# Optimization experiments

Measured on AMD Instinct MI355X. Metric: run time of the kernel, lower is better.

The kernel has to match this reference:

```python
import jax, jax.numpy as jnp
import numpy as np
from jax.scipy.special import logsumexp

B, L, S, C = 8, 2048, 2048, 256
ITERS = 20

def setup_inputs() -> dict:
    key = jax.random.key(0)
    k0, k1 = jax.random.split(key)
    feat_c0 = jax.random.normal(k0, (B, L, C), dtype=jnp.float32)
    feat_c1 = jax.random.normal(k1, (B, S, C), dtype=jnp.float32)
    bin_score = jnp.ones((), dtype=jnp.float32)  # init_bin_score = 1.0
    return {"feat_c0": feat_c0, "feat_c1": feat_c1, "bin_score": bin_score}

def _uniform_prior(b, m, n):
    # build_uniform_prior: norm = -log(m+n); log_mu/[log_nu] over augmented rows/cols
    fm, fn = jnp.float32(m), jnp.float32(n)
    norm = -jnp.log(fm + fn)
    log_mu = jnp.concatenate([jnp.full((m,), norm, jnp.float32), (jnp.log(fn) + norm)[None]])
    log_nu = jnp.concatenate([jnp.full((n,), norm, jnp.float32), (jnp.log(fm) + norm)[None]])
    log_mu = jnp.broadcast_to(log_mu[None], (b, m + 1))
    log_nu = jnp.broadcast_to(log_nu[None], (b, n + 1))
    return log_mu, log_nu, norm

def _log_sinkhorn(Z, log_mu, log_nu, iters):
    u0 = jnp.zeros_like(log_mu)
    v0 = jnp.zeros_like(log_nu)
    def body(carry, _):
        u, v = carry
        u = log_mu - logsumexp(Z + v[:, None, :], axis=2)  # [B, M+1]
        v = log_nu - logsumexp(Z + u[:, :, None], axis=1)  # [B, N+1]
        return (u, v), None
    (u, v), _ = jax.lax.scan(body, (u0, v0), None, length=iters)
    return Z + u[:, :, None] + v[:, None, :]

def reference(feat_c0, feat_c1, bin_score):
    b, m, n = feat_c0.shape[0], feat_c0.shape[1], feat_c1.shape[1]
    scores = jnp.einsum('blc,bsc->bls', feat_c0, feat_c1)  # [B, M, N]
    # augment with dustbin row/col
    bins0 = jnp.broadcast_to(bin_score, (b, m, 1))
    bins1 = jnp.broadcast_to(bin_score, (b, 1, n))
    alpha = jnp.broadcast_to(bin_score, (b, 1, 1))
    Zin = jnp.concatenate([
        jnp.concatenate([scores, bins0], axis=-1),
        jnp.concatenate([bins1, alpha], axis=-1),
    ], axis=1)  # [B, M+1, N+1]
    log_mu, log_nu, norm = _uniform_prior(b, m, n)
    Z = _log_sinkhorn(Zin, log_mu, log_nu, ITERS)
    return Z - norm
```

## Files before the change

### kernel.cpp

```cpp
#include <hip/hip_runtime.h>

#define Bn 8
#define Mn 2048
#define Nn 2048
#define Cn 256
#define Np1 2049
#define Mp1 2049
#define UVS 2056
#define SINK_ITERS 20
#define NORM   (-8.3177661667193428f)
#define LOGBIN (-0.6931471805599453f)
#define LOG2E  (1.4426950408889634f)
#define LN2    (0.6931471805599453f)
#define NORM2  (-12.0f)
#define LOGBIN2 (-1.0f)
#define PNORM  (8.3177661667193428f)

#define EXP2(x) __builtin_amdgcn_exp2f(x)
#define LOG2(x) __builtin_amdgcn_logf(x)

typedef __bf16 v8bf __attribute__((ext_vector_type(8)));
typedef float  v4f  __attribute__((ext_vector_type(4)));
typedef unsigned short v8u __attribute__((ext_vector_type(8)));

__device__ __forceinline__ float bf2f(unsigned short h){
  return __uint_as_float(((unsigned)h) << 16);
}
__device__ __forceinline__ unsigned short f2bf(float f){
  unsigned u = __float_as_uint(f);
  return (unsigned short)((u + 0x7FFFu + ((u >> 16) & 1u)) >> 16);
}
__device__ __forceinline__ float ldS(const float* p){ return *p; }
__device__ __forceinline__ float ldS(const unsigned short* p){ return bf2f(*p); }
__device__ __forceinline__ void  stS(float* p, float x){ *p = x; }
__device__ __forceinline__ void  stS(unsigned short* p, float x){ *p = f2bf(x); }

__device__ __forceinline__ void ons(float x, float& m, float& s){
  if (x <= m) { s += __expf(x - m); }
  else        { s = s * __expf(m - x) + 1.0f; m = x; }
}
__device__ __forceinline__ void comb(float& m, float& s, float m2, float s2){
  if (m2 <= m) { s += s2 * __expf(m2 - m); }
  else         { s = s * __expf(m - m2) + s2; m = m2; }
}

__global__ void __launch_bounds__(256) conv_k(
    const float* __restrict__ in, unsigned short* __restrict__ out, float scale)
{
  size_t idx = (size_t)blockIdx.x * 256 + threadIdx.x;
  const float* p = in + idx * 8;
  v4f a = *(const v4f*)p;
  v4f c = *(const v4f*)(p + 4);
  v8u o;
  #pragma unroll
  for (int e = 0; e < 4; ++e){ o[e] = f2bf(a[e] * scale); o[e+4] = f2bf(c[e] * scale); }
  *(v8u*)(out + idx * 8) = o;
}

__global__ void __launch_bounds__(256) gemm_b(
    const unsigned short* __restrict__ A, const unsigned short* __restrict__ Bm,
    unsigned short* __restrict__ S, long srow)
{
  int wid  = (blockIdx.x * 256 + threadIdx.x) >> 6;
  int lane = threadIdx.x & 63;
  int b  = wid >> 10;
  int tt = wid & 1023;
  int i0 = (tt >> 5) << 6;
  int j0 = (tt & 31) << 6;
  int ln = lane & 15, qd = lane >> 4;
  const unsigned short* Ab = A  + (size_t)b * Mn * Cn;
  const unsigned short* Bb = Bm + (size_t)b * Nn * Cn;

  v4f acc[4][4];
  #pragma unroll
  for (int r = 0; r < 4; ++r)
    #pragma unroll
    for (int c = 0; c < 4; ++c)
      #pragma unroll
      for (int e = 0; e < 4; ++e) acc[r][c][e] = 0.0f;

  #pragma unroll
  for (int k0 = 0; k0 < Cn; k0 += 32){
    int kk = k0 + qd * 8;
    v8bf af[4], bfr[4];
    #pragma unroll
    for (int r = 0; r < 4; ++r)
      af[r] = *(const v8bf*)(const void*)(Ab + (size_t)(i0 + r*16 + ln) * Cn + kk);
    #pragma unroll
    for (int c = 0; c < 4; ++c)
      bfr[c] = *(const v8bf*)(const void*)(Bb + (size_t)(j0 + c*16 + ln) * Cn + kk);
    #pragma unroll
    for (int r = 0; r < 4; ++r)
      #pragma unroll
      for (int c = 0; c < 4; ++c)
        acc[r][c] = __builtin_amdgcn_mfma_f32_16x16x32_bf16(af[r], bfr[c], acc[r][c], 0, 0, 0);
  }

  unsigned short* Sb = S + (size_t)b * Mn * Nn;
  #pragma unroll
  for (int r = 0; r < 4; ++r){
    #pragma unroll
    for (int e = 0; e < 4; ++e){
      int row = i0 + r*16 + qd*4 + e;
      #pragma unroll
      for (int c = 0; c < 4; ++c)
        Sb[(size_t)row * srow + (j0 + c*16 + ln)] = f2bf(acc[r][c][e] * LOG2E);
    }
  }
}

__global__ void __launch_bounds__(256) rmax_k(
    const unsigned short* __restrict__ S, float* __restrict__ rmax)
{
  int b = blockIdx.y, lane = threadIdx.x & 63;
  int i = blockIdx.x * 4 + (threadIdx.x >> 6);
  const unsigned short* Sr = S + ((size_t)b * Mn + i) * Nn;
  float m = -3.0e38f;
  #pragma unroll
  for (int q = 0; q < 4; ++q){
    v8u sv = *(const v8u*)(Sr + q * 512 + lane * 8);
    #pragma unroll
    for (int c = 0; c < 8; ++c) m = fmaxf(m, bf2f(sv[c]));
  }
  #pragma unroll
  for (int off = 32; off > 0; off >>= 1) m = fmaxf(m, __shfl_xor(m, off));
  if (lane == 0) rmax[(size_t)b * UVS + i] = m;
}

__global__ void __launch_bounds__(256) pass3_k(
    const unsigned short* __restrict__ S, const float* __restrict__ vin,
    float* __restrict__ uout, const float* __restrict__ rmax,
    const float* __restrict__ binp)
{
  int b = blockIdx.y, t = threadIdx.x;
  const float* vb = vin + (size_t)b * UVS;
  __shared__ float red[8];
  if (blockIdx.x < Mn / 4){
    int lane = t & 63;
    int i = blockIdx.x * 4 + (t >> 6);
    const unsigned short* Sr = S + ((size_t)b * Mn + i) * Nn;
    v4f va[8];
    #pragma unroll
    for (int q = 0; q < 4; ++q){
      int j0 = q * 512 + lane * 8;
      va[2*q]   = *(const v4f*)(vb + j0);
      va[2*q+1] = *(const v4f*)(vb + j0 + 4);
    }
    float mv = va[0][0];
    #pragma unroll
    for (int h = 0; h < 8; ++h)
      #pragma unroll
      for (int e = 0; e < 4; ++e) mv = fmaxf(mv, va[h][e]);
    #pragma unroll
    for (int off = 32; off > 0; off >>= 1) mv = fmaxf(mv, __shfl_xor(mv, off));
    float bin2 = binp[0] * LOG2E;
    float vN = vb[Nn];
    float shift = fmaxf(rmax[(size_t)b * UVS + i] + mv, bin2 + vN);
    #pragma unroll
    for (int h = 0; h < 8; ++h)
      #pragma unroll
      for (int e = 0; e < 4; ++e) va[h][e] -= shift;
    float s0 = 0.f, s1 = 0.f, s2 = 0.f, s3 = 0.f;
    #pragma unroll
    for (int q = 0; q < 4; ++q){
      v8u sv = *(const v8u*)(Sr + q * 512 + lane * 8);
      s0 += EXP2(bf2f(sv[0]) + va[2*q][0]);
      s1 += EXP2(bf2f(sv[1]) + va[2*q][1]);
      s2 += EXP2(bf2f(sv[2]) + va[2*q][2]);
      s3 += EXP2(bf2f(sv[3]) + va[2*q][3]);
      s0 += EXP2(bf2f(sv[4]) + va[2*q+1][0]);
      s1 += EXP2(bf2f(sv[5]) + va[2*q+1][1]);
      s2 += EXP2(bf2f(sv[6]) + va[2*q+1][2]);
      s3 += EXP2(bf2f(sv[7]) + va[2*q+1][3]);
    }
    float s = (s0 + s1) + (s2 + s3);
    #pragma unroll
    for (int off = 32; off > 0; off >>= 1) s += __shfl_xor(s, off);
    if (lane == 0){
      s += EXP2(bin2 + vN - shift);
      uout[(size_t)b * UVS + i] = NORM2 - (shift + LOG2(s));
    }
  } else {
    float x[9];
    #pragma unroll
    for (int k = 0; k < 9; ++k){
      int j = t + k * 256;
      x[k] = (j <= Nn) ? vb[j] : -3.0e38f;
    }
    float m = x[0];
    #pragma unroll
    for (int k = 1; k < 9; ++k) m = fmaxf(m, x[k]);
    #pragma unroll
    for (int off = 32; off > 0; off >>= 1) m = fmaxf(m, __shfl_down(m, off));
    int w = t >> 6;
    if ((t & 63) == 0) red[w] = m;
    __syncthreads();
    float M = fmaxf(fmaxf(red[0], red[1]), fmaxf(red[2], red[3]));
    float s = 0.0f;
    #pragma unroll
    for (int k = 0; k < 9; ++k) s += EXP2(x[k] - M);
    #pragma unroll
    for (int off = 32; off > 0; off >>= 1) s += __shfl_down(s, off);
    __syncthreads();
    if ((t & 63) == 0) red[w] = s;
    __syncthreads();
    if (t == 0){
      float Ss = red[0] + red[1] + red[2] + red[3];
      float bin2 = binp[0] * LOG2E;
      uout[(size_t)b * UVS + Mn] = LOGBIN2 - (bin2 + M + LOG2(Ss));
    }
  }
}

__global__ void __launch_bounds__(256) final2_k(
    const unsigned short* __restrict__ S, float* __restrict__ out,
    const float* __restrict__ u, const float* __restrict__ v,
    const float* __restrict__ binp)
{
  int i = blockIdx.x, b = blockIdx.y, t = threadIdx.x;
  float bin2 = binp[0] * LOG2E;
  const float* vb = v + (size_t)b * UVS;
  float ui = u[(size_t)b * UVS + i];
  float* ob = out + ((size_t)b * Mp1 + i) * Np1;
  if (i < Mn){
    const unsigned short* Sr = S + ((size_t)b * Mn + i) * Nn;
    int j0 = t * 8;
    v8u sv = *(const v8u*)(Sr + j0);
    v4f va = *(const v4f*)(vb + j0);
    v4f vc = *(const v4f*)(vb + j0 + 4);
    #pragma unroll
    for (int c = 0; c < 4; ++c) ob[j0 + c]     = (bf2f(sv[c])   + ui + va[c]) * LN2 + PNORM;
    #pragma unroll
    for (int c = 0; c < 4; ++c) ob[j0 + 4 + c] = (bf2f(sv[c+4]) + ui + vc[c]) * LN2 + PNORM;
    if (t == 0) ob[Nn] = (bin2 + ui + vb[Nn]) * LN2 + PNORM;
  } else {
    for (int j = t; j <= Nn; j += 256) ob[j] = (bin2 + ui + vb[j]) * LN2 + PNORM;
  }
}

template<typename ST>
__global__ void __launch_bounds__(256) gemm_k(
    const float* __restrict__ A, const float* __restrict__ Bm,
    ST* __restrict__ S, long srow, long sbatch)
{
  int wid  = (blockIdx.x * 256 + threadIdx.x) >> 6;
  int lane = threadIdx.x & 63;
  int b  = wid >> 10;
  int tt = wid & 1023;
  int i0 = (tt >> 5) << 6;
  int j0 = (tt & 31) << 6;
  int ln = lane & 15, qd = lane >> 4;
  const float* Ab = A  + (size_t)b * Mn * Cn;
  const float* Bb = Bm + (size_t)b * Nn * Cn;

  v4f acc[4][4];
  #pragma unroll
  for (int r = 0; r < 4; ++r)
    #pragma unroll
    for (int c = 0; c < 4; ++c)
      #pragma unroll
      for (int e = 0; e < 4; ++e) acc[r][c][e] = 0.0f;

  #pragma unroll
  for (int k0 = 0; k0 < Cn; k0 += 32){
    int kk = k0 + qd * 8;
    v8bf af[4], bfr[4];
    #pragma unroll
    for (int r = 0; r < 4; ++r){
      const float* p = Ab + (size_t)(i0 + r*16 + ln) * Cn + kk;
      v4f lo = *(const v4f*)p, hi = *(const v4f*)(p + 4);
      #pragma unroll
      for (int e = 0; e < 4; ++e){ af[r][e] = (__bf16)lo[e]; af[r][e+4] = (__bf16)hi[e]; }
    }
    #pragma unroll
    for (int c = 0; c < 4; ++c){
      const float* p = Bb + (size_t)(j0 + c*16 + ln) * Cn + kk;
      v4f lo = *(const v4f*)p, hi = *(const v4f*)(p + 4);
      #pragma unroll
      for (int e = 0; e < 4; ++e){ bfr[c][e] = (__bf16)lo[e]; bfr[c][e+4] = (__bf16)hi[e]; }
    }
    #pragma unroll
    for (int r = 0; r < 4; ++r)
      #pragma unroll
      for (int c = 0; c < 4; ++c)
        acc[r][c] = __builtin_amdgcn_mfma_f32_16x16x32_bf16(af[r], bfr[c], acc[r][c], 0, 0, 0);
  }

  ST* Sb = S + (size_t)b * sbatch;
  #pragma unroll
  for (int r = 0; r < 4; ++r){
    #pragma unroll
    for (int e = 0; e < 4; ++e){
      int row = i0 + r*16 + qd*4 + e;
      #pragma unroll
      for (int c = 0; c < 4; ++c)
        stS(Sb + (size_t)row * srow + (j0 + c*16 + ln), acc[r][c][e]);
    }
  }
}

__global__ void __launch_bounds__(256) row_pass_t(
    const unsigned short* __restrict__ S, const float* __restrict__ vin,
    float* __restrict__ uout, const float* __restrict__ binp)
{
  int b = blockIdx.y, t = threadIdx.x;
  const float* vb = vin + (size_t)b * UVS;
  __shared__ float red[8];
  if (blockIdx.x < Mn / 4){
    int lane = t & 63;
    int i = blockIdx.x * 4 + (t >> 6);
    const unsigned short* Sr = S + ((size_t)b * Mn + i) * Nn;
    float x[32];
    #pragma unroll
    for (int q = 0; q < 4; ++q){
      int j0 = q * 512 + lane * 8;
      v8u sv = *(const v8u*)(Sr + j0);
      v4f va = *(const v4f*)(vb + j0);
      v4f vc = *(const v4f*)(vb + j0 + 4);
      #pragma unroll
      for (int c = 0; c < 4; ++c){
        x[q*8 + c]     = bf2f(sv[c])   + va[c];
        x[q*8 + 4 + c] = bf2f(sv[c+4]) + vc[c];
      }
    }
    float mx[16];
    #pragma unroll
    for (int k = 0; k < 16; ++k) mx[k] = fmaxf(x[2*k], x[2*k+1]);
    #pragma unroll
    for (int k = 0; k < 8; ++k) mx[k] = fmaxf(mx[k], mx[k+8]);
    #pragma unroll
    for (int k = 0; k < 4; ++k) mx[k] = fmaxf(mx[k], mx[k+4]);
    float m = fmaxf(fmaxf(mx[0], mx[1]), fmaxf(mx[2], mx[3]));
    #pragma unroll
    for (int off = 32; off > 0; off >>= 1) m = fmaxf(m, __shfl_xor(m, off));
    float s0 = 0.f, s1 = 0.f, s2 = 0.f, s3 = 0.f;
    #pragma unroll
    for (int k = 0; k < 8; ++k){
      s0 += __expf(x[4*k]     - m);
      s1 += __expf(x[4*k + 1] - m);
      s2 += __expf(x[4*k + 2] - m);
      s3 += __expf(x[4*k + 3] - m);
    }
    float s = (s0 + s1) + (s2 + s3);
    #pragma unroll
    for (int off = 32; off > 0; off >>= 1) s += __shfl_xor(s, off);
    if (lane == 0){
      float M = m, Ss = s;
      comb(M, Ss, binp[0] + vb[Nn], 1.0f);
      uout[(size_t)b * UVS + i] = NORM - (M + __logf(Ss));
    }
  } else {
    float x[9];
    #pragma unroll
    for (int k = 0; k < 9; ++k){
      int j = t + k * 256;
      x[k] = (j <= Nn) ? vb[j] : -3.0e38f;
    }
    float m = x[0];
    #pragma unroll
    for (int k = 1; k < 9; ++k) m = fmaxf(m, x[k]);
    #pragma unroll
    for (int off = 32; off > 0; off >>= 1) m = fmaxf(m, __shfl_down(m, off));
    int w = t >> 6;
    if ((t & 63) == 0) red[w] = m;
    __syncthreads();
    float M = fmaxf(fmaxf(red[0], red[1]), fmaxf(red[2], red[3]));
    float s = 0.0f;
    #pragma unroll
    for (int k = 0; k < 9; ++k) s += __expf(x[k] - M);
    #pragma unroll
    for (int off = 32; off > 0; off >>= 1) s += __shfl_down(s, off);
    __syncthreads();
    if ((t & 63) == 0) red[w] = s;
    __syncthreads();
    if (t == 0){
      float Ss = red[0] + red[1] + red[2] + red[3];
      uout[(size_t)b * UVS + Mn] = LOGBIN - (binp[0] + M + __logf(Ss));
    }
  }
}

__global__ void __launch_bounds__(256) row_pass_v(
    const unsigned short* __restrict__ S, const float* __restrict__ v,
    float* __restrict__ u, const float* __restrict__ binp)
{
  int i = blockIdx.x, b = blockIdx.y, t = threadIdx.x;
  const float* vb = v + (size_t)b * UVS;
  float x[9];
  int K;
  if (i < Mn){
    const unsigned short* Sr = S + ((size_t)b * Mn + i) * Nn;
    int j0 = t * 8;
    v8u sv = *(const v8u*)(Sr + j0);
    v4f va = *(const v4f*)(vb + j0);
    v4f vc = *(const v4f*)(vb + j0 + 4);
    #pragma unroll
    for (int c = 0; c < 4; ++c){ x[c] = bf2f(sv[c]) + va[c]; x[c+4] = bf2f(sv[c+4]) + vc[c]; }
    K = 8;
  } else {
    #pragma unroll
    for (int k = 0; k < 9; ++k){
      int j = t + k * 256;
      x[k] = (j <= Nn) ? vb[j] : -3.0e38f;
    }
    K = 9;
  }
  float m = x[0];
  #pragma unroll
  for (int k = 1; k < 9; ++k) if (k < K) m = fmaxf(m, x[k]);
  #pragma unroll
  for (int off = 32; off > 0; off >>= 1) m = fmaxf(m, __shfl_down(m, off));
  __shared__ float red[8];
  int w = t >> 6;
  if ((t & 63) == 0) red[w] = m;
  __syncthreads();
  float M = fmaxf(fmaxf(red[0], red[1]), fmaxf(red[2], red[3]));
  float s = 0.0f;
  #pragma unroll
  for (int k = 0; k < 9; ++k) if (k < K) s += __expf(x[k] - M);
  #pragma unroll
  for (int off = 32; off > 0; off >>= 1) s += __shfl_down(s, off);
  __syncthreads();
  if ((t & 63) == 0) red[w] = s;
  __syncthreads();
  if (t == 0){
    float Ss = red[0] + red[1] + red[2] + red[3];
    float bin = binp[0];
    if (i < Mn){
      comb(M, Ss, bin + vb[Nn], 1.0f);
      u[(size_t)b * UVS + i] = NORM - (M + __logf(Ss));
    } else {
      u[(size_t)b * UVS + Mn] = LOGBIN - (bin + M + __logf(Ss));
    }
  }
}

__global__ void __launch_bounds__(256) col_pass_v(
    const unsigned short* __restrict__ S, const float* __restrict__ u,
    float* __restrict__ v, const float* __restrict__ binp)
{
  int blk = blockIdx.x, b = blockIdx.y, t = threadIdx.x;
  const float* ub = u + (size_t)b * UVS;
  __shared__ float lm[32][65];
  __shared__ float ls[32][65];
  __shared__ float red[16];
  if (blk < Nn / 64){
    int tx = t & 7, ty = t >> 3;
    int j0 = blk * 64 + tx * 8;
    const unsigned short* Sb = S + (size_t)b * Mn * Nn;
    float m[8], s[8];
    #pragma unroll
    for (int c = 0; c < 8; ++c){ m[c] = -3.0e38f; s[c] = 0.0f; }
    for (int i = ty; i < Mn; i += 32){
      v8u sv = *(const v8u*)(Sb + (size_t)i * Nn + j0);
      float ui = ub[i];
      #pragma unroll
      for (int c = 0; c < 8; ++c){
        float x  = bf2f(sv[c]) + ui;
        float mn = fmaxf(m[c], x);
        s[c] = s[c] * __expf(m[c] - mn) + __expf(x - mn);
        m[c] = mn;
      }
    }
    #pragma unroll
    for (int c = 0; c < 8; ++c){ lm[ty][tx*8 + c] = m[c]; ls[ty][tx*8 + c] = s[c]; }
    __syncthreads();
    if (t < 64){
      float M = -3.0e38f, Ss = 0.0f;
      #pragma unroll 4
      for (int rg = 0; rg < 32; ++rg) comb(M, Ss, lm[rg][t], ls[rg][t]);
      float bin = binp[0];
      comb(M, Ss, bin + ub[Mn], 1.0f);
      v[(size_t)b * UVS + blk * 64 + t] = NORM - (M + __logf(Ss));
    }
  } else {
    float x[9];
    #pragma unroll
    for (int k = 0; k < 9; ++k){
      int j = t + k * 256;
      x[k] = (j <= Mn) ? ub[j] : -3.0e38f;
    }
    float m = x[0];
    #pragma unroll
    for (int k = 1; k < 9; ++k) m = fmaxf(m, x[k]);
    #pragma unroll
    for (int off = 32; off > 0; off >>= 1) m = fmaxf(m, __shfl_down(m, off));
    int w = t >> 6;
    if ((t & 63) == 0) red[w] = m;
    __syncthreads();
    float M = fmaxf(fmaxf(red[0], red[1]), fmaxf(red[2], red[3]));
    float s = 0.0f;
    #pragma unroll
    for (int k = 0; k < 9; ++k) s += __expf(x[k] - M);
    #pragma unroll
    for (int off = 32; off > 0; off >>= 1) s += __shfl_down(s, off);
    __syncthreads();
    if ((t & 63) == 0) red[w] = s;
    __syncthreads();
    if (t == 0){
      float Ss = red[0] + red[1] + red[2] + red[3];
      float bin = binp[0];
      v[(size_t)b * UVS + Nn] = LOGBIN - (bin + M + __logf(Ss));
    }
  }
}

__global__ void __launch_bounds__(256) final_v(
    const unsigned short* __restrict__ S, float* __restrict__ out,
    const float* __restrict__ u, const float* __restrict__ v,
    const float* __restrict__ binp)
{
  int i = blockIdx.x, b = blockIdx.y, t = threadIdx.x;
  float bin = binp[0];
  const float* vb = v + (size_t)b * UVS;
  float ui = u[(size_t)b * UVS + i];
  float* ob = out + ((size_t)b * Mp1 + i) * Np1;
  if (i < Mn){
    const unsigned short* Sr = S + ((size_t)b * Mn + i) * Nn;
    int j0 = t * 8;
    v8u sv = *(const v8u*)(Sr + j0);
    v4f va = *(const v4f*)(vb + j0);
    v4f vc = *(const v4f*)(vb + j0 + 4);
    #pragma unroll
    for (int c = 0; c < 4; ++c) ob[j0 + c]     = bf2f(sv[c])   + ui + va[c] - NORM;
    #pragma unroll
    for (int c = 0; c < 4; ++c) ob[j0 + 4 + c] = bf2f(sv[c+4]) + ui + vc[c] - NORM;
    if (t == 0) ob[Nn] = bin + ui + vb[Nn] - NORM;
  } else {
    for (int j = t; j <= Nn; j += 256) ob[j] = bin + ui + vb[j] - NORM;
  }
}

template<typename ST>
__global__ void __launch_bounds__(256) row_pass(
    const ST* __restrict__ S, long srow, long sbatch,
    const float* __restrict__ v, float* __restrict__ u,
    const float* __restrict__ binp)
{
  int i = blockIdx.x, b = blockIdx.y, t = threadIdx.x;
  const float* vb = v + (size_t)b * UVS;
  float m = -3.0e38f, s = 0.0f;
  if (i < Mn){
    const ST* Sr = S + (size_t)b * sbatch + (size_t)i * srow;
    #pragma unroll
    for (int jj = 0; jj < Nn / 256; ++jj){
      int j = jj * 256 + t;
      ons(ldS(Sr + j) + vb[j], m, s);
    }
  } else {
    for (int j = t; j <= Nn; j += 256) ons(vb[j], m, s);
  }
  #pragma unroll
  for (int off = 32; off > 0; off >>= 1){
    float m2 = __shfl_down(m, off);
    float s2 = __shfl_down(s, off);
    comb(m, s, m2, s2);
  }
  __shared__ float sm[4], ss[4];
  int w = t >> 6;
  if ((t & 63) == 0){ sm[w] = m; ss[w] = s; }
  __syncthreads();
  if (t == 0){
    #pragma unroll
    for (int w2 = 1; w2 < 4; ++w2) comb(m, s, sm[w2], ss[w2]);
    float bin = binp[0];
    if (i < Mn){
      comb(m, s, bin + vb[Nn], 1.0f);
      u[(size_t)b * UVS + i] = NORM - (m + __logf(s));
    } else {
      u[(size_t)b * UVS + Mn] = LOGBIN - (bin + m + __logf(s));
    }
  }
}

template<typename ST>
__global__ void __launch_bounds__(1024) col_pass(
    const ST* __restrict__ S, long srow, long sbatch,
    const float* __restrict__ u, float* __restrict__ v,
    const float* __restrict__ binp)
{
  int jt = blockIdx.x, b = blockIdx.y, t = threadIdx.x;
  const float* ub = u + (size_t)b * UVS;
  __shared__ float sm[16][64];
  __shared__ float ss[16][64];
  if (jt < Nn / 64){
    int c = t & 63, rg = t >> 6;
    int j = jt * 64 + c;
    const ST* Sc = S + (size_t)b * sbatch + j;
    float m = -3.0e38f, s = 0.0f;
    #pragma unroll 8
    for (int i = rg; i < Mn; i += 16)
      ons(ldS(Sc + (size_t)i * srow) + ub[i], m, s);
    sm[rg][c] = m; ss[rg][c] = s;
    __syncthreads();
    if (rg == 0){
      #pragma unroll
      for (int r = 1; r < 16; ++r) comb(m, s, sm[r][c], ss[r][c]);
      float bin = binp[0];
      comb(m, s, bin + ub[Mn], 1.0f);
      v[(size_t)b * UVS + j] = NORM - (m + __logf(s));
    }
  } else {
    float m = -3.0e38f, s = 0.0f;
    for (int i = t; i <= Mn; i += 1024) ons(ub[i], m, s);
    #pragma unroll
    for (int off = 32; off > 0; off >>= 1){
      float m2 = __shfl_down(m, off);
      float s2 = __shfl_down(s, off);
      comb(m, s, m2, s2);
    }
    int w = t >> 6;
    if ((t & 63) == 0){ sm[0][w] = m; ss[0][w] = s; }
    __syncthreads();
    if (t == 0){
      #pragma unroll
      for (int w2 = 1; w2 < 16; ++w2) comb(m, s, sm[0][w2], ss[0][w2]);
      float bin = binp[0];
      v[(size_t)b * UVS + Nn] = LOGBIN - (bin + m + __logf(s));
    }
  }
}

template<typename ST>
__global__ void __launch_bounds__(256) final_k(
    const ST* __restrict__ S, long srow, long sbatch,
    float* __restrict__ out, const float* __restrict__ u,
    const float* __restrict__ v, const float* __restrict__ binp)
{
  int i = blockIdx.x, b = blockIdx.y, t = threadIdx.x;
  float bin = binp[0];
  float ui = u[(size_t)b * UVS + i];
  const float* vb = v + (size_t)b * UVS;
  float* ob = out + ((size_t)b * Mp1 + i) * Np1;
  if (i < Mn){
    const ST* Sr = S + (size_t)b * sbatch + (size_t)i * srow;
    for (int j = t; j < Nn; j += 256)
      ob[j] = ldS(Sr + j) + ui + vb[j] - NORM;
    if (t == 0) ob[Nn] = bin + ui + vb[Nn] - NORM;
  } else {
    for (int j = t; j <= Nn; j += 256)
      ob[j] = bin + ui + vb[j] - NORM;
  }
}

__global__ void zero_uv(float* uv){
  int t = blockIdx.x * 256 + threadIdx.x;
  if (t < 2 * Bn * UVS) uv[t] = 0.0f;
}

extern "C" void kernel_launch(void* const* d_in, const int* in_sizes, int n_in,
                              void* d_out, int out_size, void* d_ws, size_t ws_size,
                              hipStream_t stream)
{
  const float* A    = (const float*)d_in[0];
  const float* Bm   = (const float*)d_in[1];
  const float* binp = (const float*)d_in[2];
  float* out = (float*)d_out;

  const size_t S_bytes  = (size_t)Bn * Mn * Nn * 2;
  const size_t AB_bytes = (size_t)Bn * Mn * Cn * 2;
  const size_t uv_bytes = (size_t)4 * Bn * UVS * 4;
  bool useT2 = ws_size >= 2 * S_bytes + 2 * AB_bytes + uv_bytes;
  bool useT  = ws_size >= 2 * S_bytes + 2 * (size_t)Bn * UVS * 4;
  bool useW  = ws_size >= S_bytes + 2 * (size_t)Bn * UVS * 4;

  float* u;
  unsigned short* Sw  = nullptr;
  unsigned short* STw = nullptr;
  unsigned short* Abf = nullptr;
  unsigned short* Bbf = nullptr;
  if (useT2){
    Sw  = (unsigned short*)d_ws;
    STw = (unsigned short*)((char*)d_ws + S_bytes);
    Abf = (unsigned short*)((char*)d_ws + 2 * S_bytes);
    Bbf = (unsigned short*)((char*)d_ws + 2 * S_bytes + AB_bytes);
    u   = (float*)((char*)d_ws + 2 * S_bytes + 2 * AB_bytes);
  } else if (useT){
    Sw  = (unsigned short*)d_ws;
    STw = (unsigned short*)((char*)d_ws + S_bytes);
    u   = (float*)((char*)d_ws + 2 * S_bytes);
  } else if (useW){
    Sw = (unsigned short*)d_ws;
    u  = (float*)((char*)d_ws + S_bytes);
  } else {
    u  = (float*)d_ws;
  }
  float* v = u + (size_t)Bn * UVS;

  zero_uv<<<(2 * Bn * UVS + 255) / 256, 256, 0, stream>>>(u);

  if (useT2){
    float* rmaxS = v + (size_t)Bn * UVS;
    float* rmaxT = rmaxS + (size_t)Bn * UVS;
    const int cgrid = (Bn * Mn * Cn / 8) / 256;
    conv_k<<<cgrid, 256, 0, stream>>>(A,  Abf, 1.0f);
    conv_k<<<cgrid, 256, 0, stream>>>(Bm, Bbf, 1.0f);
    gemm_b<<<(Bn * 32 * 32) / 4, 256, 0, stream>>>(Abf, Bbf, Sw,  Nn);
    gemm_b<<<(Bn * 32 * 32) / 4, 256, 0, stream>>>(Bbf, Abf, STw, Mn);
    rmax_k<<<dim3(Mn / 4, Bn), 256, 0, stream>>>(Sw,  rmaxS);
    rmax_k<<<dim3(Nn / 4, Bn), 256, 0, stream>>>(STw, rmaxT);
    for (int it = 0; it < SINK_ITERS; ++it){
      pass3_k<<<dim3(Mn / 4 + 1, Bn), 256, 0, stream>>>(Sw,  v, u, rmaxS, binp);
      pass3_k<<<dim3(Nn / 4 + 1, Bn), 256, 0, stream>>>(STw, u, v, rmaxT, binp);
    }
    final2_k<<<dim3(Mp1, Bn), 256, 0, stream>>>(Sw, out, u, v, binp);
  } else if (useT){
    gemm_k<unsigned short><<<(Bn * 32 * 32) / 4, 256, 0, stream>>>(A, Bm, Sw,  Nn, (long)Mn * Nn);
    gemm_k<unsigned short><<<(Bn * 32 * 32) / 4, 256, 0, stream>>>(Bm, A, STw, Mn, (long)Mn * Nn);
    for (int it = 0; it < SINK_ITERS; ++it){
      row_pass_t<<<dim3(Mn / 4 + 1, Bn), 256, 0, stream>>>(Sw,  v, u, binp);
      row_pass_t<<<dim3(Nn / 4 + 1, Bn), 256, 0, stream>>>(STw, u, v, binp);
    }
    final_v<<<dim3(Mp1, Bn), 256, 0, stream>>>(Sw, out, u, v, binp);
  } else if (useW){
    gemm_k<unsigned short><<<(Bn * 32 * 32) / 4, 256, 0, stream>>>(A, Bm, Sw, Nn, (long)Mn * Nn);
    for (int it = 0; it < SINK_ITERS; ++it){
      row_pass_v<<<dim3(Mp1, Bn), 256, 0, stream>>>(Sw, v, u, binp);
      col_pass_v<<<dim3(Nn / 64 + 1, Bn), 256, 0, stream>>>(Sw, u, v, binp);
    }
    final_v<<<dim3(Mp1, Bn), 256, 0, stream>>>(Sw, out, u, v, binp);
  } else {
    const long srow = Np1, sbatch = (long)Mp1 * Np1;
    gemm_k<float><<<(Bn * 32 * 32) / 4, 256, 0, stream>>>(A, Bm, out, srow, sbatch);
    for (int it = 0; it < SINK_ITERS; ++it){
      row_pass<float><<<dim3(Mp1, Bn), 256, 0, stream>>>(out, srow, sbatch, v, u, binp);
      col_pass<float><<<dim3(Nn / 64 + 1, Bn), 1024, 0, stream>>>(out, srow, sbatch, u, v, binp);
    }
    final_k<float><<<dim3(Mp1, Bn), 256, 0, stream>>>(out, srow, sbatch, out, u, v, binp);
  }
}
```

Baseline: 793.4 us.

## Fuse transposed score write into GEMM and process two rows per wave in Sinkhorn passes

The GEMM kernel now writes both the score matrix and its transpose, staging each wave's 64x64 tile in shared memory, so the second GEMM launch (which recomputed the same products) is dropped. The Sinkhorn pass kernel handles two rows per wavefront, reusing the loaded v vector and its max reduction across both rows and halving the block count. This trades extra LDS usage and strided transposed stores (64-element runs) for removing a full GEMM and some redundant vector loads per iteration.

```diff
diff --git a/kernel.cpp b/kernel.cpp
--- a/kernel.cpp
+++ b/kernel.cpp
@@ -57,11 +57,13 @@
   *(v8u*)(out + idx * 8) = o;
 }
 
-__global__ void __launch_bounds__(256) gemm_b(
+__global__ void __launch_bounds__(256) gemm_bt(
     const unsigned short* __restrict__ A, const unsigned short* __restrict__ Bm,
-    unsigned short* __restrict__ S, long srow)
-{
+    unsigned short* __restrict__ S, unsigned short* __restrict__ ST)
+{
+  __shared__ unsigned short lt[4][64][65];
   int wid  = (blockIdx.x * 256 + threadIdx.x) >> 6;
+  int w    = (threadIdx.x >> 6) & 3;
   int lane = threadIdx.x & 63;
   int b  = wid >> 10;
   int tt = wid & 1023;
@@ -101,10 +103,26 @@
   for (int r = 0; r < 4; ++r){
     #pragma unroll
     for (int e = 0; e < 4; ++e){
-      int row = i0 + r*16 + qd*4 + e;
-      #pragma unroll
-      for (int c = 0; c < 4; ++c)
-        Sb[(size_t)row * srow + (j0 + c*16 + ln)] = f2bf(acc[r][c][e] * LOG2E);
+      int lr = r*16 + qd*4 + e;
+      #pragma unroll
+      for (int c = 0; c < 4; ++c){
+        unsigned short hv = f2bf(acc[r][c][e] * LOG2E);
+        Sb[(size_t)(i0 + lr) * Nn + (j0 + c*16 + ln)] = hv;
+        lt[w][lr][c*16 + ln] = hv;
+      }
+    }
+  }
+  unsigned short* Tb = ST + (size_t)b * Mn * Nn;
+  #pragma unroll
+  for (int r = 0; r < 4; ++r){
+    #pragma unroll
+    for (int e = 0; e < 4; ++e){
+      int p = r*16 + qd*4 + e;
+      #pragma unroll
+      for (int c = 0; c < 4; ++c){
+        int q = c*16 + ln;
+        Tb[(size_t)(j0 + p) * Mn + (i0 + q)] = lt[w][q][p];
+      }
     }
   }
 }
@@ -127,7 +145,7 @@
   if (lane == 0) rmax[(size_t)b * UVS + i] = m;
 }
 
-__global__ void __launch_bounds__(256) pass3_k(
+__global__ void __launch_bounds__(256) pass4_k(
     const unsigned short* __restrict__ S, const float* __restrict__ vin,
     float* __restrict__ uout, const float* __restrict__ rmax,
     const float* __restrict__ binp)
@@ -135,10 +153,9 @@
   int b = blockIdx.y, t = threadIdx.x;
   const float* vb = vin + (size_t)b * UVS;
   __shared__ float red[8];
-  if (blockIdx.x < Mn / 4){
-    int lane = t & 63;
-    int i = blockIdx.x * 4 + (t >> 6);
-    const unsigned short* Sr = S + ((size_t)b * Mn + i) * Nn;
+  if (blockIdx.x < Mn / 8){
+    int lane = t & 63, wv = t >> 6;
+    int i0 = blockIdx.x * 8 + wv * 2;
     v4f va[8];
     #pragma unroll
     for (int q = 0; q < 4; ++q){
@@ -154,31 +171,48 @@
     #pragma unroll
     for (int off = 32; off > 0; off >>= 1) mv = fmaxf(mv, __shfl_xor(mv, off));
     float bin2 = binp[0] * LOG2E;
-    float vN = vb[Nn];
-    float shift = fmaxf(rmax[(size_t)b * UVS + i] + mv, bin2 + vN);
-    #pragma unroll
-    for (int h = 0; h < 8; ++h)
-      #pragma unroll
-      for (int e = 0; e < 4; ++e) va[h][e] -= shift;
-    float s0 = 0.f, s1 = 0.f, s2 = 0.f, s3 = 0.f;
+    float vN  = vb[Nn];
+    float bvn = bin2 + vN;
+    float sh0 = fmaxf(rmax[(size_t)b * UVS + i0]     + mv, bvn);
+    float sh1 = fmaxf(rmax[(size_t)b * UVS + i0 + 1] + mv, bvn);
+    const unsigned short* Sr0 = S + ((size_t)b * Mn + i0) * Nn;
+    const unsigned short* Sr1 = Sr0 + Nn;
+    float a0=0.f,a1=0.f,a2=0.f,a3=0.f;
+    float c0=0.f,c1=0.f,c2=0.f,c3=0.f;
     #pragma unroll
     for (int q = 0; q < 4; ++q){
-      v8u sv = *(const v8u*)(Sr + q * 512 + lane * 8);
-      s0 += EXP2(bf2f(sv[0]) + va[2*q][0]);
-      s1 += EXP2(bf2f(sv[1]) + va[2*q][1]);
-      s2 += EXP2(bf2f(sv[2]) + va[2*q][2]);
-      s3 += EXP2(bf2f(sv[3]) + va[2*q][3]);
-      s0 += EXP2(bf2f(sv[4]) + va[2*q+1][0]);
-      s1 += EXP2(bf2f(sv[5]) + va[2*q+1][1]);
-      s2 += EXP2(bf2f(sv[6]) + va[2*q+1][2]);
-      s3 += EXP2(bf2f(sv[7]) + va[2*q+1][3]);
-    }
-    float s = (s0 + s1) + (s2 + s3);
-    #pragma unroll
-    for (int off = 32; off > 0; off >>= 1) s += __shfl_xor(s, off);
+      int j0 = q * 512 + lane * 8;
+      v8u r0 = *(const v8u*)(Sr0 + j0);
+      v8u r1 = *(const v8u*)(Sr1 + j0);
+      a0 += EXP2(bf2f(r0[0]) + va[2*q][0]   - sh0);
+      a1 += EXP2(bf2f(r0[1]) + va[2*q][1]   - sh0);
+      a2 += EXP2(bf2f(r0[2]) + va[2*q][2]   - sh0);
+      a3 += EXP2(bf2f(r0[3]) + va[2*q][3]   - sh0);
+      c0 += EXP2(bf2f(r1[0]) + va[2*q][0]   - sh1);
+      c1 += EXP2(bf2f(r1[1]) + va[2*q][1]   - sh1);
+      c2 += EXP2(bf2f(r1[2]) + va[2*q][2]   - sh1);
+      c3 += EXP2(bf2f(r1[3]) + va[2*q][3]   - sh1);
+      a0 += EXP2(bf2f(r0[4]) + va[2*q+1][0] - sh0);
+      a1 += EXP2(bf2f(r0[5]) + va[2*q+1][1] - sh0);
+      a2 += EXP2(bf2f(r0[6]) + va[2*q+1][2] - sh0);
+      a3 += EXP2(bf2f(r0[7]) + va[2*q+1][3] - sh0);
+      c0 += EXP2(bf2f(r1[4]) + va[2*q+1][0] - sh1);
+      c1 += EXP2(bf2f(r1[5]) + va[2*q+1][1] - sh1);
+      c2 += EXP2(bf2f(r1[6]) + va[2*q+1][2] - sh1);
+      c3 += EXP2(bf2f(r1[7]) + va[2*q+1][3] - sh1);
+    }
+    float sA = (a0 + a1) + (a2 + a3);
+    float sB = (c0 + c1) + (c2 + c3);
+    #pragma unroll
+    for (int off = 32; off > 0; off >>= 1){
+      sA += __shfl_xor(sA, off);
+      sB += __shfl_xor(sB, off);
+    }
     if (lane == 0){
-      s += EXP2(bin2 + vN - shift);
-      uout[(size_t)b * UVS + i] = NORM2 - (shift + LOG2(s));
+      sA += EXP2(bvn - sh0);
+      sB += EXP2(bvn - sh1);
+      uout[(size_t)b * UVS + i0]     = NORM2 - (sh0 + LOG2(sA));
+      uout[(size_t)b * UVS + i0 + 1] = NORM2 - (sh1 + LOG2(sB));
     }
   } else {
     float x[9];
@@ -695,13 +729,12 @@
     const int cgrid = (Bn * Mn * Cn / 8) / 256;
     conv_k<<<cgrid, 256, 0, stream>>>(A,  Abf, 1.0f);
     conv_k<<<cgrid, 256, 0, stream>>>(Bm, Bbf, 1.0f);
-    gemm_b<<<(Bn * 32 * 32) / 4, 256, 0, stream>>>(Abf, Bbf, Sw,  Nn);
-    gemm_b<<<(Bn * 32 * 32) / 4, 256, 0, stream>>>(Bbf, Abf, STw, Mn);
+    gemm_bt<<<(Bn * 32 * 32) / 4, 256, 0, stream>>>(Abf, Bbf, Sw, STw);
     rmax_k<<<dim3(Mn / 4, Bn), 256, 0, stream>>>(Sw,  rmaxS);
     rmax_k<<<dim3(Nn / 4, Bn), 256, 0, stream>>>(STw, rmaxT);
     for (int it = 0; it < SINK_ITERS; ++it){
-      pass3_k<<<dim3(Mn / 4 + 1, Bn), 256, 0, stream>>>(Sw,  v, u, rmaxS, binp);
-      pass3_k<<<dim3(Nn / 4 + 1, Bn), 256, 0, stream>>>(STw, u, v, rmaxT, binp);
+      pass4_k<<<dim3(Mn / 8 + 1, Bn), 256, 0, stream>>>(Sw,  v, u, rmaxS, binp);
+      pass4_k<<<dim3(Nn / 8 + 1, Bn), 256, 0, stream>>>(STw, u, v, rmaxT, binp);
     }
     final2_k<<<dim3(Mp1, Bn), 256, 0, stream>>>(Sw, out, u, v, binp);
   } else if (useT){
```

Measured after the change: 745.3 us. 1.06x faster.
